# Performance work log

Measured on AMD Instinct MI355X. Metric: run time of the kernel, lower is better.

The kernel has to match this reference:

```python
import jax, jax.numpy as jnp
import numpy as np

NUM_EXPERTS = 8
TOP_K = 2
HIDDEN = 2048
INTER = 1408
TOKENS = 4096


def setup_inputs() -> dict:
    key = jax.random.key(0)
    ks = jax.random.split(key, 5)
    scale_h = 1.0 / np.sqrt(HIDDEN)
    scale_i = 1.0 / np.sqrt(INTER)
    return {
        "x": jax.random.normal(ks[0], (TOKENS, HIDDEN), dtype=jnp.float32),
        "router_w": jax.random.normal(ks[1], (NUM_EXPERTS, HIDDEN), dtype=jnp.float32) * scale_h,
        "w_gate": jax.random.normal(ks[2], (NUM_EXPERTS, HIDDEN, INTER), dtype=jnp.float32) * scale_h,
        "w_up": jax.random.normal(ks[3], (NUM_EXPERTS, HIDDEN, INTER), dtype=jnp.float32) * scale_h,
        "w_down": jax.random.normal(ks[4], (NUM_EXPERTS, INTER, HIDDEN), dtype=jnp.float32) * scale_i,
    }


def reference(x, router_w, w_gate, w_up, w_down):
    # Router: softmax over experts, top-k, renormalize top-k probs
    logits = x @ router_w.T                       # [T, E]
    probs = jax.nn.softmax(logits, axis=-1)
    top_vals, top_idx = jax.lax.top_k(probs, TOP_K)  # [T, K]
    top_vals = top_vals / jnp.sum(top_vals, axis=-1, keepdims=True)
    # Combine weights: [T, E], zero for unselected experts
    t_ar = jnp.arange(x.shape[0])[:, None]
    combine = jnp.zeros((x.shape[0], NUM_EXPERTS), dtype=x.dtype).at[t_ar, top_idx].add(top_vals)
    # Expert SwiGLU FFN: down( silu(x@gate) * (x@up) ), weighted combine.
    # Loop over the small fixed expert set (8); each iteration is a dense GEMM chain.
    out = jnp.zeros_like(x)
    for e in range(NUM_EXPERTS):
        h = jax.nn.silu(x @ w_gate[e]) * (x @ w_up[e])  # [T, INTER]
        out = out + combine[:, e:e + 1] * (h @ w_down[e])
    return out
```

## Files before the change

### kernel.cpp

```cpp
#include <hip/hip_runtime.h>
#include <hip/hip_bf16.h>
#include <cstdint>
#include <cstddef>

#define TOKENS 4096
#define HIDDEN 2048
#define INTER  1408
#define NE     8
#define NGU    2816
#define CAP_ROWS 9216

typedef __bf16 bf16;
typedef __bf16 bf16x8 __attribute__((ext_vector_type(8)));
typedef float  f32x4  __attribute__((ext_vector_type(4)));

__device__ __forceinline__ void async16(const void* g, void* l) {
  __builtin_amdgcn_global_load_lds((const __attribute__((address_space(1))) void*)g,
                                   (__attribute__((address_space(3))) void*)l,
                                   16, 0, 0);
}

__global__ void router_kernel(const float* __restrict__ x, const float* __restrict__ rw,
                              bf16* __restrict__ xb, int* __restrict__ cnt,
                              int* __restrict__ tok, float* __restrict__ wts) {
  const int w = threadIdx.x >> 6, l = threadIdx.x & 63;
  const int t = blockIdx.x * 4 + w;
  const float4* x4 = (const float4*)(x + (size_t)t * HIDDEN);
  const float4* r4 = (const float4*)rw;
  float acc[NE];
#pragma unroll
  for (int e = 0; e < NE; ++e) acc[e] = 0.f;
#pragma unroll
  for (int c = 0; c < 8; ++c) {
    const int idx = c * 64 + l;
    const float4 v = x4[idx];
    bf16* dst = xb + (size_t)t * HIDDEN + idx * 4;
    dst[0] = (bf16)v.x; dst[1] = (bf16)v.y; dst[2] = (bf16)v.z; dst[3] = (bf16)v.w;
#pragma unroll
    for (int e = 0; e < NE; ++e) {
      const float4 u = r4[e * 512 + idx];
      acc[e] += v.x * u.x + v.y * u.y + v.z * u.z + v.w * u.w;
    }
  }
#pragma unroll
  for (int e = 0; e < NE; ++e)
#pragma unroll
    for (int s = 32; s > 0; s >>= 1) acc[e] += __shfl_xor(acc[e], s, 64);
  if (l == 0) {
    int i0 = 0; float l0 = acc[0];
#pragma unroll
    for (int e = 1; e < NE; ++e) if (acc[e] > l0) { l0 = acc[e]; i0 = e; }
    int i1 = -1; float l1 = -3.4e38f;
#pragma unroll
    for (int e = 0; e < NE; ++e) if (e != i0 && acc[e] > l1) { l1 = acc[e]; i1 = e; }
    const float w0 = 1.f / (1.f + __expf(l1 - l0));
    const float w1 = 1.f - w0;
    int p = atomicAdd(&cnt[i0], 1); tok[i0 * 4096 + p] = t; wts[i0 * 4096 + p] = w0;
    p = atomicAdd(&cnt[i1], 1);     tok[i1 * 4096 + p] = t; wts[i1 * 4096 + p] = w1;
  }
}

__global__ void scan_kernel(const int* __restrict__ cnt, int* __restrict__ offs) {
  if (threadIdx.x == 0 && blockIdx.x == 0) {
    int o = 0;
    for (int e = 0; e < NE; ++e) { offs[e] = o; o += ((cnt[e] + 127) >> 7) << 7; }
    offs[NE] = o;
  }
}

__global__ __launch_bounds__(256) void transpose64(
    const float* __restrict__ in, bf16* __restrict__ out, int R, int C,
    size_t inSlab, size_t outSlab, int mode) {
  __shared__ float tile[64][68];
  in  += blockIdx.z * inSlab;
  out += blockIdx.z * outSlab;
  const int c0 = blockIdx.x * 64, r0 = blockIdx.y * 64;
  const int t = threadIdx.x;
  const int row = t >> 4, cq = t & 15;
  const float* src = in + (size_t)(r0 + row) * C + c0 + cq * 4;
#pragma unroll
  for (int p = 0; p < 4; ++p) {
    const float4 v = *(const float4*)(src + (size_t)(p * 16) * C);
    *(float4*)&tile[p * 16 + row][cq * 4] = v;
  }
  __syncthreads();
  const int oc = t >> 2, rq = t & 3;
  float vals[16];
#pragma unroll
  for (int i = 0; i < 16; ++i) vals[i] = tile[rq * 16 + i][oc];
  const int c = c0 + oc;
  int p;
  if (mode == 0) p = c;
  else p = ((c >> 4) << 5) + (c & 15) + (mode == 2 ? 16 : 0);
  bf16x8 o0, o1;
#pragma unroll
  for (int i = 0; i < 8; ++i) { o0[i] = (bf16)vals[i]; o1[i] = (bf16)vals[8 + i]; }
  bf16* dst = out + (size_t)p * R + r0 + rq * 16;
  *(bf16x8*)dst = o0;
  *(bf16x8*)(dst + 8) = o1;
}

__global__ __launch_bounds__(256, 4) void gemm_gateup(
    const bf16* __restrict__ X, const bf16* __restrict__ W, bf16* __restrict__ H,
    const int* __restrict__ cnt, const int* __restrict__ offs,
    const int* __restrict__ tok, const float* __restrict__ wts) {
  const int e = blockIdx.z, mt = blockIdx.y, nt = blockIdx.x;
  const int c = cnt[e];
  if (mt * 128 >= c) return;

  __shared__ bf16 sA[128 * 32];
  __shared__ bf16 sB[128 * 32];

  const int t = threadIdx.x, l = t & 63, w = t >> 6;
  const int iA0 = t, iA1 = t + 256;
  const int rA0 = iA0 >> 2, g0 = iA0 & 3;
  const int rA1 = iA1 >> 2, g1 = iA1 & 3;
  const int gr0 = tok[e * 4096 + (mt * 128 + rA0 < c ? mt * 128 + rA0 : c - 1)];
  const int gr1 = tok[e * 4096 + (mt * 128 + rA1 < c ? mt * 128 + rA1 : c - 1)];
  const bf16* pa0 = X + (size_t)gr0 * HIDDEN + g0 * 8;
  const bf16* pa1 = X + (size_t)gr1 * HIDDEN + g1 * 8;
  const bf16* pb0 = W + ((size_t)e * NGU + nt * 128 + rA0) * HIDDEN + g0 * 8;
  const bf16* pb1 = W + ((size_t)e * NGU + nt * 128 + rA1) * HIDDEN + g1 * 8;
  bf16* la0 = sA + iA0 * 8; bf16* la1 = sA + iA1 * 8;
  bf16* lb0 = sB + iA0 * 8; bf16* lb1 = sB + iA1 * 8;

  const int wm = (w >> 1) * 64, wn = (w & 1) * 64;
  const int r16 = l & 15, quad = l >> 4;
  const bf16* fA = sA + (wm + r16) * 32 + quad * 8;
  const bf16* fB = sB + (wn + r16) * 32 + quad * 8;

  f32x4 acc[4][4];
#pragma unroll
  for (int i = 0; i < 4; ++i)
#pragma unroll
    for (int j = 0; j < 4; ++j) acc[i][j] = (f32x4){0.f, 0.f, 0.f, 0.f};

  for (int kk = 0; kk < HIDDEN; kk += 32) {
    async16(pa0 + kk, la0); async16(pa1 + kk, la1);
    async16(pb0 + kk, lb0); async16(pb1 + kk, lb1);
    __syncthreads();
    bf16x8 a[4], b[4];
#pragma unroll
    for (int i = 0; i < 4; ++i) a[i] = *(const bf16x8*)(fA + i * 16 * 32);
#pragma unroll
    for (int j = 0; j < 4; ++j) b[j] = *(const bf16x8*)(fB + j * 16 * 32);
#pragma unroll
    for (int i = 0; i < 4; ++i)
#pragma unroll
      for (int j = 0; j < 4; ++j)
        acc[i][j] = __builtin_amdgcn_mfma_f32_16x16x32_bf16(a[i], b[j], acc[i][j], 0, 0, 0);
    __syncthreads();
  }

  const int mLoc = mt * 128 + wm + quad * 4;
  const int hcol = nt * 64 + (wn >> 1) + r16;
#pragma unroll
  for (int i = 0; i < 4; ++i)
#pragma unroll
    for (int r = 0; r < 4; ++r) {
      const int m = mLoc + i * 16 + r;
      const int mc = m < c ? m : c - 1;
      const float ws = wts[e * 4096 + mc];
      const float g0v = acc[i][0][r], u0v = acc[i][1][r];
      const float g1v = acc[i][2][r], u1v = acc[i][3][r];
      const float h0 = (g0v / (1.f + __expf(-g0v))) * u0v * ws;
      const float h1 = (g1v / (1.f + __expf(-g1v))) * u1v * ws;
      bf16* dst = H + (size_t)(offs[e] + m) * INTER + hcol;
      dst[0]  = (bf16)h0;
      dst[16] = (bf16)h1;
    }
}

__global__ __launch_bounds__(256, 4) void gemm_down(
    const bf16* __restrict__ Hin, const bf16* __restrict__ W, float* __restrict__ out,
    const int* __restrict__ cnt, const int* __restrict__ offs,
    const int* __restrict__ tok) {
  const int e = blockIdx.z, mt = blockIdx.y, nt = blockIdx.x;
  const int c = cnt[e];
  if (mt * 128 >= c) return;

  __shared__ bf16 sA[128 * 32];
  __shared__ bf16 sB[128 * 32];

  const int t = threadIdx.x, l = t & 63, w = t >> 6;
  const int iA0 = t, iA1 = t + 256;
  const int rA0 = iA0 >> 2, g0 = iA0 & 3;
  const int rA1 = iA1 >> 2, g1 = iA1 & 3;
  const int base = offs[e] + mt * 128;
  const bf16* pa0 = Hin + (size_t)(base + rA0) * INTER + g0 * 8;
  const bf16* pa1 = Hin + (size_t)(base + rA1) * INTER + g1 * 8;
  const bf16* pb0 = W + ((size_t)e * HIDDEN + nt * 128 + rA0) * INTER + g0 * 8;
  const bf16* pb1 = W + ((size_t)e * HIDDEN + nt * 128 + rA1) * INTER + g1 * 8;
  bf16* la0 = sA + iA0 * 8; bf16* la1 = sA + iA1 * 8;
  bf16* lb0 = sB + iA0 * 8; bf16* lb1 = sB + iA1 * 8;

  const int wm = (w >> 1) * 64, wn = (w & 1) * 64;
  const int r16 = l & 15, quad = l >> 4;
  const bf16* fA = sA + (wm + r16) * 32 + quad * 8;
  const bf16* fB = sB + (wn + r16) * 32 + quad * 8;

  f32x4 acc[4][4];
#pragma unroll
  for (int i = 0; i < 4; ++i)
#pragma unroll
    for (int j = 0; j < 4; ++j) acc[i][j] = (f32x4){0.f, 0.f, 0.f, 0.f};

  for (int kk = 0; kk < INTER; kk += 32) {
    async16(pa0 + kk, la0); async16(pa1 + kk, la1);
    async16(pb0 + kk, lb0); async16(pb1 + kk, lb1);
    __syncthreads();
    bf16x8 a[4], b[4];
#pragma unroll
    for (int i = 0; i < 4; ++i) a[i] = *(const bf16x8*)(fA + i * 16 * 32);
#pragma unroll
    for (int j = 0; j < 4; ++j) b[j] = *(const bf16x8*)(fB + j * 16 * 32);
#pragma unroll
    for (int i = 0; i < 4; ++i)
#pragma unroll
      for (int j = 0; j < 4; ++j)
        acc[i][j] = __builtin_amdgcn_mfma_f32_16x16x32_bf16(a[i], b[j], acc[i][j], 0, 0, 0);
    __syncthreads();
  }

  const int mBase = mt * 128 + wm + quad * 4;
  const int colBase = nt * 128 + wn + r16;
#pragma unroll
  for (int i = 0; i < 4; ++i)
#pragma unroll
    for (int r = 0; r < 4; ++r) {
      const int m = mBase + i * 16 + r;
      if (m < c) {
        const int tkn = tok[e * 4096 + m];
        float* dst = out + (size_t)tkn * HIDDEN + colBase;
#pragma unroll
        for (int j = 0; j < 4; ++j) atomicAdd(dst + j * 16, acc[i][j][r]);
      }
    }
}

extern "C" void kernel_launch(void* const* d_in, const int* in_sizes, int n_in,
                              void* d_out, int out_size, void* d_ws, size_t ws_size,
                              hipStream_t stream) {
  const float* x  = (const float*)d_in[0];
  const float* rw = (const float*)d_in[1];
  const float* wg = (const float*)d_in[2];
  const float* wu = (const float*)d_in[3];
  const float* wd = (const float*)d_in[4];
  float* out = (float*)d_out;

  char* ws = (char*)d_ws;
  size_t o = 0;
  auto alloc = [&](size_t b) { void* p = ws + o; o += (b + 255) & ~(size_t)255; return p; };
  int*   cnt  = (int*)alloc(NE * 4);
  int*   offs = (int*)alloc((NE + 1) * 4);
  int*   tok  = (int*)alloc((size_t)NE * 4096 * 4);
  float* wts  = (float*)alloc((size_t)NE * 4096 * 4);
  bf16*  xb   = (bf16*)alloc((size_t)TOKENS * HIDDEN * 2);
  bf16*  wgu  = (bf16*)alloc((size_t)NE * NGU * HIDDEN * 2);
  bf16*  wdt  = (bf16*)alloc((size_t)NE * HIDDEN * INTER * 2);
  bf16*  h    = (bf16*)alloc((size_t)CAP_ROWS * INTER * 2);

  hipMemsetAsync(cnt, 0, NE * 4, stream);
  hipMemsetAsync(d_out, 0, (size_t)TOKENS * HIDDEN * 4, stream);

  router_kernel<<<TOKENS / 4, 256, 0, stream>>>(x, rw, xb, cnt, tok, wts);
  scan_kernel<<<1, 64, 0, stream>>>(cnt, offs);

  transpose64<<<dim3(INTER / 64, HIDDEN / 64, NE), 256, 0, stream>>>(
      wg, wgu, HIDDEN, INTER, (size_t)HIDDEN * INTER, (size_t)NGU * HIDDEN, 1);
  transpose64<<<dim3(INTER / 64, HIDDEN / 64, NE), 256, 0, stream>>>(
      wu, wgu, HIDDEN, INTER, (size_t)HIDDEN * INTER, (size_t)NGU * HIDDEN, 2);
  transpose64<<<dim3(HIDDEN / 64, INTER / 64, NE), 256, 0, stream>>>(
      wd, wdt, INTER, HIDDEN, (size_t)INTER * HIDDEN, (size_t)HIDDEN * INTER, 0);

  gemm_gateup<<<dim3(NGU / 128, TOKENS / 128, NE), 256, 0, stream>>>(
      xb, wgu, h, cnt, offs, tok, wts);
  gemm_down<<<dim3(HIDDEN / 128, TOKENS / 128, NE), 256, 0, stream>>>(
      h, wdt, out, cnt, offs, tok);
}
```

Before: 697.8 us.

## Replace atomic scatter with bf16 staging plus gather-combine; merge transposes; double K-step

The down GEMM no longer scatters into the fp32 output with atomicAdd. It writes bf16 rows to a per-slot buffer, and a new combine kernel uses an inverse slot map from the router to gather each token's two rows and sum them. This drops the output memset and the atomic contention, at the cost of an extra bf16 buffer round trip and rounding the partial sums to bf16. The three weight transposes are merged into one launch, with some out-of-range blocks exiting early. Both GEMMs now load 64 K per barrier pair, halving the number of syncs.

```diff
diff --git a/kernel.cpp b/kernel.cpp
--- a/kernel.cpp
+++ b/kernel.cpp
@@ -9,6 +9,7 @@
 #define NE     8
 #define NGU    2816
 #define CAP_ROWS 9216
+#define LDSA   (128 * 32)
 
 typedef __bf16 bf16;
 typedef __bf16 bf16x8 __attribute__((ext_vector_type(8)));
@@ -20,9 +21,10 @@
                                    16, 0, 0);
 }
 
-__global__ void router_kernel(const float* __restrict__ x, const float* __restrict__ rw,
-                              bf16* __restrict__ xb, int* __restrict__ cnt,
-                              int* __restrict__ tok, float* __restrict__ wts) {
+__global__ void k_router(const float* __restrict__ x, const float* __restrict__ rw,
+                         bf16* __restrict__ xb, int* __restrict__ cnt,
+                         int* __restrict__ tok, float* __restrict__ wts,
+                         int* __restrict__ inv) {
   const int w = threadIdx.x >> 6, l = threadIdx.x & 63;
   const int t = blockIdx.x * 4 + w;
   const float4* x4 = (const float4*)(x + (size_t)t * HIDDEN);
@@ -55,12 +57,14 @@
     for (int e = 0; e < NE; ++e) if (e != i0 && acc[e] > l1) { l1 = acc[e]; i1 = e; }
     const float w0 = 1.f / (1.f + __expf(l1 - l0));
     const float w1 = 1.f - w0;
-    int p = atomicAdd(&cnt[i0], 1); tok[i0 * 4096 + p] = t; wts[i0 * 4096 + p] = w0;
-    p = atomicAdd(&cnt[i1], 1);     tok[i1 * 4096 + p] = t; wts[i1 * 4096 + p] = w1;
-  }
-}
-
-__global__ void scan_kernel(const int* __restrict__ cnt, int* __restrict__ offs) {
+    int p = atomicAdd(&cnt[i0], 1);
+    tok[i0 * 4096 + p] = t; wts[i0 * 4096 + p] = w0; inv[2 * t] = (i0 << 12) | p;
+    p = atomicAdd(&cnt[i1], 1);
+    tok[i1 * 4096 + p] = t; wts[i1 * 4096 + p] = w1; inv[2 * t + 1] = (i1 << 12) | p;
+  }
+}
+
+__global__ void k_scan(const int* __restrict__ cnt, int* __restrict__ offs) {
   if (threadIdx.x == 0 && blockIdx.x == 0) {
     int o = 0;
     for (int e = 0; e < NE; ++e) { offs[e] = o; o += ((cnt[e] + 127) >> 7) << 7; }
@@ -68,13 +72,29 @@
   }
 }
 
-__global__ __launch_bounds__(256) void transpose64(
-    const float* __restrict__ in, bf16* __restrict__ out, int R, int C,
-    size_t inSlab, size_t outSlab, int mode) {
+__global__ __launch_bounds__(256) void k_tr(
+    const float* __restrict__ wg, const float* __restrict__ wu,
+    const float* __restrict__ wd, bf16* __restrict__ wgu, bf16* __restrict__ wdt) {
+  const int z = blockIdx.z;
+  int mode, R, C;
+  const float* in; bf16* out;
+  if (z < 16) {
+    mode = (z < 8) ? 1 : 2;
+    const int e = z & 7;
+    in = (z < 8 ? wg : wu) + (size_t)e * HIDDEN * INTER;
+    out = wgu + (size_t)e * NGU * HIDDEN;
+    R = HIDDEN; C = INTER;
+  } else {
+    mode = 0;
+    const int e = z - 16;
+    in = wd + (size_t)e * INTER * HIDDEN;
+    out = wdt + (size_t)e * HIDDEN * INTER;
+    R = INTER; C = HIDDEN;
+  }
+  const int c0 = blockIdx.x * 64, r0 = blockIdx.y * 64;
+  if (c0 >= C || r0 >= R) return;
+
   __shared__ float tile[64][68];
-  in  += blockIdx.z * inSlab;
-  out += blockIdx.z * outSlab;
-  const int c0 = blockIdx.x * 64, r0 = blockIdx.y * 64;
   const int t = threadIdx.x;
   const int row = t >> 4, cq = t & 15;
   const float* src = in + (size_t)(r0 + row) * C + c0 + cq * 4;
@@ -100,7 +120,7 @@
   *(bf16x8*)(dst + 8) = o1;
 }
 
-__global__ __launch_bounds__(256, 4) void gemm_gateup(
+__global__ __launch_bounds__(256, 4) void k_gu(
     const bf16* __restrict__ X, const bf16* __restrict__ W, bf16* __restrict__ H,
     const int* __restrict__ cnt, const int* __restrict__ offs,
     const int* __restrict__ tok, const float* __restrict__ wts) {
@@ -108,8 +128,8 @@
   const int c = cnt[e];
   if (mt * 128 >= c) return;
 
-  __shared__ bf16 sA[128 * 32];
-  __shared__ bf16 sB[128 * 32];
+  __shared__ bf16 sA[2 * LDSA];
+  __shared__ bf16 sB[2 * LDSA];
 
   const int t = threadIdx.x, l = t & 63, w = t >> 6;
   const int iA0 = t, iA1 = t + 256;
@@ -135,20 +155,27 @@
 #pragma unroll
     for (int j = 0; j < 4; ++j) acc[i][j] = (f32x4){0.f, 0.f, 0.f, 0.f};
 
-  for (int kk = 0; kk < HIDDEN; kk += 32) {
-    async16(pa0 + kk, la0); async16(pa1 + kk, la1);
-    async16(pb0 + kk, lb0); async16(pb1 + kk, lb1);
+  for (int kk = 0; kk < HIDDEN; kk += 64) {
+    async16(pa0 + kk, la0);      async16(pa1 + kk, la1);
+    async16(pb0 + kk, lb0);      async16(pb1 + kk, lb1);
+    async16(pa0 + kk + 32, la0 + LDSA); async16(pa1 + kk + 32, la1 + LDSA);
+    async16(pb0 + kk + 32, lb0 + LDSA); async16(pb1 + kk + 32, lb1 + LDSA);
     __syncthreads();
-    bf16x8 a[4], b[4];
-#pragma unroll
-    for (int i = 0; i < 4; ++i) a[i] = *(const bf16x8*)(fA + i * 16 * 32);
-#pragma unroll
-    for (int j = 0; j < 4; ++j) b[j] = *(const bf16x8*)(fB + j * 16 * 32);
-#pragma unroll
-    for (int i = 0; i < 4; ++i)
-#pragma unroll
-      for (int j = 0; j < 4; ++j)
-        acc[i][j] = __builtin_amdgcn_mfma_f32_16x16x32_bf16(a[i], b[j], acc[i][j], 0, 0, 0);
+#pragma unroll
+    for (int s = 0; s < 2; ++s) {
+      const bf16* fAs = fA + s * LDSA;
+      const bf16* fBs = fB + s * LDSA;
+      bf16x8 a[4], b[4];
+#pragma unroll
+      for (int i = 0; i < 4; ++i) a[i] = *(const bf16x8*)(fAs + i * 16 * 32);
+#pragma unroll
+      for (int j = 0; j < 4; ++j) b[j] = *(const bf16x8*)(fBs + j * 16 * 32);
+#pragma unroll
+      for (int i = 0; i < 4; ++i)
+#pragma unroll
+        for (int j = 0; j < 4; ++j)
+          acc[i][j] = __builtin_amdgcn_mfma_f32_16x16x32_bf16(a[i], b[j], acc[i][j], 0, 0, 0);
+    }
     __syncthreads();
   }
 
@@ -171,16 +198,15 @@
     }
 }
 
-__global__ __launch_bounds__(256, 4) void gemm_down(
-    const bf16* __restrict__ Hin, const bf16* __restrict__ W, float* __restrict__ out,
-    const int* __restrict__ cnt, const int* __restrict__ offs,
-    const int* __restrict__ tok) {
+__global__ __launch_bounds__(256, 4) void k_dn(
+    const bf16* __restrict__ Hin, const bf16* __restrict__ W, bf16* __restrict__ O2,
+    const int* __restrict__ cnt, const int* __restrict__ offs) {
   const int e = blockIdx.z, mt = blockIdx.y, nt = blockIdx.x;
   const int c = cnt[e];
   if (mt * 128 >= c) return;
 
-  __shared__ bf16 sA[128 * 32];
-  __shared__ bf16 sB[128 * 32];
+  __shared__ bf16 sA[2 * LDSA];
+  __shared__ bf16 sB[2 * LDSA];
 
   const int t = threadIdx.x, l = t & 63, w = t >> 6;
   const int iA0 = t, iA1 = t + 256;
@@ -205,37 +231,59 @@
 #pragma unroll
     for (int j = 0; j < 4; ++j) acc[i][j] = (f32x4){0.f, 0.f, 0.f, 0.f};
 
-  for (int kk = 0; kk < INTER; kk += 32) {
-    async16(pa0 + kk, la0); async16(pa1 + kk, la1);
-    async16(pb0 + kk, lb0); async16(pb1 + kk, lb1);
+  for (int kk = 0; kk < INTER; kk += 64) {
+    async16(pa0 + kk, la0);      async16(pa1 + kk, la1);
+    async16(pb0 + kk, lb0);      async16(pb1 + kk, lb1);
+    async16(pa0 + kk + 32, la0 + LDSA); async16(pa1 + kk + 32, la1 + LDSA);
+    async16(pb0 + kk + 32, lb0 + LDSA); async16(pb1 + kk + 32, lb1 + LDSA);
     __syncthreads();
-    bf16x8 a[4], b[4];
-#pragma unroll
-    for (int i = 0; i < 4; ++i) a[i] = *(const bf16x8*)(fA + i * 16 * 32);
-#pragma unroll
-    for (int j = 0; j < 4; ++j) b[j] = *(const bf16x8*)(fB + j * 16 * 32);
-#pragma unroll
-    for (int i = 0; i < 4; ++i)
-#pragma unroll
-      for (int j = 0; j < 4; ++j)
-        acc[i][j] = __builtin_amdgcn_mfma_f32_16x16x32_bf16(a[i], b[j], acc[i][j], 0, 0, 0);
+#pragma unroll
+    for (int s = 0; s < 2; ++s) {
+      const bf16* fAs = fA + s * LDSA;
+      const bf16* fBs = fB + s * LDSA;
+      bf16x8 a[4], b[4];
+#pragma unroll
+      for (int i = 0; i < 4; ++i) a[i] = *(const bf16x8*)(fAs + i * 16 * 32);
+#pragma unroll
+      for (int j = 0; j < 4; ++j) b[j] = *(const bf16x8*)(fBs + j * 16 * 32);
+#pragma unroll
+      for (int i = 0; i < 4; ++i)
+#pragma unroll
+        for (int j = 0; j < 4; ++j)
+          acc[i][j] = __builtin_amdgcn_mfma_f32_16x16x32_bf16(a[i], b[j], acc[i][j], 0, 0, 0);
+    }
     __syncthreads();
   }
 
-  const int mBase = mt * 128 + wm + quad * 4;
+  const int rowBase = offs[e] + mt * 128 + wm + quad * 4;
   const int colBase = nt * 128 + wn + r16;
 #pragma unroll
   for (int i = 0; i < 4; ++i)
 #pragma unroll
     for (int r = 0; r < 4; ++r) {
-      const int m = mBase + i * 16 + r;
-      if (m < c) {
-        const int tkn = tok[e * 4096 + m];
-        float* dst = out + (size_t)tkn * HIDDEN + colBase;
-#pragma unroll
-        for (int j = 0; j < 4; ++j) atomicAdd(dst + j * 16, acc[i][j][r]);
-      }
-    }
+      bf16* dst = O2 + (size_t)(rowBase + i * 16 + r) * HIDDEN + colBase;
+#pragma unroll
+      for (int j = 0; j < 4; ++j) dst[j * 16] = (bf16)acc[i][j][r];
+    }
+}
+
+__global__ void k_cb(const bf16* __restrict__ O2, const int* __restrict__ inv,
+                     const int* __restrict__ offs, float* __restrict__ out) {
+  const int t = blockIdx.x;
+  const int col = threadIdx.x * 8;
+  const int s0 = inv[2 * t], s1 = inv[2 * t + 1];
+  const int r0 = offs[s0 >> 12] + (s0 & 4095);
+  const int r1 = offs[s1 >> 12] + (s1 & 4095);
+  const bf16x8 a = *(const bf16x8*)(O2 + (size_t)r0 * HIDDEN + col);
+  const bf16x8 b = *(const bf16x8*)(O2 + (size_t)r1 * HIDDEN + col);
+  float4 o0, o1;
+  o0.x = (float)a[0] + (float)b[0]; o0.y = (float)a[1] + (float)b[1];
+  o0.z = (float)a[2] + (float)b[2]; o0.w = (float)a[3] + (float)b[3];
+  o1.x = (float)a[4] + (float)b[4]; o1.y = (float)a[5] + (float)b[5];
+  o1.z = (float)a[6] + (float)b[6]; o1.w = (float)a[7] + (float)b[7];
+  float* dst = out + (size_t)t * HIDDEN + col;
+  *(float4*)dst = o0;
+  *(float4*)(dst + 4) = o1;
 }
 
 extern "C" void kernel_launch(void* const* d_in, const int* in_sizes, int n_in,
@@ -255,26 +303,19 @@
   int*   offs = (int*)alloc((NE + 1) * 4);
   int*   tok  = (int*)alloc((size_t)NE * 4096 * 4);
   float* wts  = (float*)alloc((size_t)NE * 4096 * 4);
+  int*   inv  = (int*)alloc((size_t)TOKENS * 2 * 4);
   bf16*  xb   = (bf16*)alloc((size_t)TOKENS * HIDDEN * 2);
   bf16*  wgu  = (bf16*)alloc((size_t)NE * NGU * HIDDEN * 2);
   bf16*  wdt  = (bf16*)alloc((size_t)NE * HIDDEN * INTER * 2);
   bf16*  h    = (bf16*)alloc((size_t)CAP_ROWS * INTER * 2);
+  bf16*  o2   = (bf16*)alloc((size_t)CAP_ROWS * HIDDEN * 2);
 
   hipMemsetAsync(cnt, 0, NE * 4, stream);
-  hipMemsetAsync(d_out, 0, (size_t)TOKENS * HIDDEN * 4, stream);
-
-  router_kernel<<<TOKENS / 4, 256, 0, stream>>>(x, rw, xb, cnt, tok, wts);
-  scan_kernel<<<1, 64, 0, stream>>>(cnt, offs);
-
-  transpose64<<<dim3(INTER / 64, HIDDEN / 64, NE), 256, 0, stream>>>(
-      wg, wgu, HIDDEN, INTER, (size_t)HIDDEN * INTER, (size_t)NGU * HIDDEN, 1);
-  transpose64<<<dim3(INTER / 64, HIDDEN / 64, NE), 256, 0, stream>>>(
-      wu, wgu, HIDDEN, INTER, (size_t)HIDDEN * INTER, (size_t)NGU * HIDDEN, 2);
-  transpose64<<<dim3(HIDDEN / 64, INTER / 64, NE), 256, 0, stream>>>(
-      wd, wdt, INTER, HIDDEN, (size_t)INTER * HIDDEN, (size_t)HIDDEN * INTER, 0);
-
-  gemm_gateup<<<dim3(NGU / 128, TOKENS / 128, NE), 256, 0, stream>>>(
-      xb, wgu, h, cnt, offs, tok, wts);
-  gemm_down<<<dim3(HIDDEN / 128, TOKENS / 128, NE), 256, 0, stream>>>(
-      h, wdt, out, cnt, offs, tok);
-}
+
+  k_router<<<TOKENS / 4, 256, 0, stream>>>(x, rw, xb, cnt, tok, wts, inv);
+  k_scan<<<1, 64, 0, stream>>>(cnt, offs);
+  k_tr<<<dim3(32, 32, 24), 256, 0, stream>>>(wg, wu, wd, wgu, wdt);
+  k_gu<<<dim3(NGU / 128, TOKENS / 128, NE), 256, 0, stream>>>(xb, wgu, h, cnt, offs, tok, wts);
+  k_dn<<<dim3(HIDDEN / 128, TOKENS / 128, NE), 256, 0, stream>>>(h, wdt, o2, cnt, offs);
+  k_cb<<<TOKENS, 256, 0, stream>>>(o2, inv, offs, out);
+}
```

Result: no change. 704.3 us (+0.9%).
